# Performance work log

Hardware: AMD Instinct MI355X
Metric: run time of the kernel (lower is better)

The kernel has to match this reference:

```python
import jax, jax.numpy as jnp
import numpy as np

B = 64        # batch
N = 1024      # num_nodes
D_IN = 2      # input feature dim per node
U = 64        # num_units (hidden)
K = 2         # max_diffusion_step


def setup_inputs() -> dict:
    key = jax.random.key(0)
    ks = jax.random.split(key, 8)
    inputs = jax.random.normal(ks[0], (B, N * D_IN), dtype=jnp.float32)
    hx = jax.random.normal(ks[1], (B, N * U), dtype=jnp.float32)
    # random-walk style supports: nonnegative, row-normalized -> stable Chebyshev recursion
    a0 = jax.random.uniform(ks[2], (N, N), dtype=jnp.float32)
    a1 = jax.random.uniform(ks[3], (N, N), dtype=jnp.float32)
    support0 = a0 / jnp.sum(a0, axis=1, keepdims=True)
    support1 = a1 / jnp.sum(a1, axis=1, keepdims=True)
    num_matrices = 2 * K + 1            # len(supports)*K + 1 = 5
    in_sz = (D_IN + U) * num_matrices   # 330
    # xavier-normal init
    std_o = float(np.sqrt(2.0 / (in_sz + 2 * U)))
    std_u = float(np.sqrt(2.0 / (in_sz + U)))
    weights_output = jax.random.normal(ks[4], (in_sz, 2 * U), dtype=jnp.float32) * std_o
    weights_update = jax.random.normal(ks[5], (in_sz, U), dtype=jnp.float32) * std_u
    biases_output = jnp.ones((2 * U,), dtype=jnp.float32)
    biases_update = jnp.zeros((U,), dtype=jnp.float32)
    return {"inputs": inputs, "hx": hx, "support0": support0, "support1": support1,
            "weights_output": weights_output, "biases_output": biases_output,
            "weights_update": weights_update, "biases_update": biases_update}


def _gconv(x_cat, supports, W, b, out_size):
    # x_cat: [B, N, F]  -> Chebyshev diffusion series then dense projection
    Bsz, Nn, F = x_cat.shape
    x0 = x_cat.transpose(1, 2, 0).reshape(Nn, F * Bsz)  # [N, F*B]
    xs = [x0]
    for S in supports:
        x1 = S @ x0
        xs.append(x1)
        xk1, xk2 = x1, x0
        for _ in range(2, K + 1):
            x2 = 2.0 * (S @ xk1) - xk2
            xs.append(x2)
            xk1, xk2 = x2, xk1
    M = len(xs)                                         # num_matrices
    x = jnp.stack(xs, axis=0)                           # [M, N, F*B]
    x = x.reshape(M, Nn, F, Bsz).transpose(3, 1, 2, 0)  # [B, N, F, M]
    x = x.reshape(Bsz * Nn, F * M)
    y = x @ W + b                                       # [B*N, out_size]
    return y.reshape(Bsz, Nn * out_size)


def reference(inputs, hx, support0, support1, weights_output, biases_output,
              weights_update, biases_update):
    supports = (support0, support1)
    xi = inputs.reshape(B, N, D_IN)
    hs = hx.reshape(B, N, U)
    cat = jnp.concatenate([xi, hs], axis=2)             # [B, N, D_IN+U]
    value = jax.nn.sigmoid(_gconv(cat, supports, weights_output, biases_output, 2 * U))
    value = value.reshape(B, N, 2 * U)
    r = value[..., :U].reshape(B, N * U)
    u = value[..., U:].reshape(B, N * U)
    cat2 = jnp.concatenate([xi, (r * hx).reshape(B, N, U)], axis=2)
    c = jnp.tanh(_gconv(cat2, supports, weights_update, biases_update, U))
    return u * hx + (1.0 - u) * c
```

## Files before the change

kernel.cpp:

```cpp
#include <hip/hip_runtime.h>


typedef unsigned short u16;
typedef unsigned int u32;
typedef short s16x8 __attribute__((ext_vector_type(8)));
typedef float f32x4 __attribute__((ext_vector_type(4)));
typedef u16 u16x4 __attribute__((ext_vector_type(4)));

#define NN 1024
#define NB 64
#define NF 66
#define NCOLS 4224
#define KPAD 352
#define ASTRIDE 360

__device__ __forceinline__ u16 f2bf(float f) {
  u32 u = __builtin_bit_cast(u32, f);
  u = (u + 0x7fffu + ((u >> 16) & 1u)) >> 16;
  return (u16)u;
}
__device__ __forceinline__ float bf2f(u16 h) {
  u32 u = ((u32)h) << 16;
  return __builtin_bit_cast(float, u);
}

__device__ __forceinline__ void gload16(const void* g, void* l) {
  __builtin_amdgcn_global_load_lds(
      (const __attribute__((address_space(1))) u32*)g,
      (__attribute__((address_space(3))) u32*)l, 16, 0, 0);
}

#define CHEB_WAIT(N)                                   \
  do {                                                 \
    asm volatile("s_waitcnt vmcnt(" #N ")" ::: "memory"); \
    __builtin_amdgcn_s_barrier();                      \
    asm volatile("" ::: "memory");                     \
  } while (0)


__global__ __launch_bounds__(256) void pack_supports(
    const float* __restrict__ s0, const float* __restrict__ s1,
    u16* __restrict__ d0, u16* __restrict__ d1) {
  int i = (blockIdx.x * 256 + threadIdx.x) * 4;
  f32x4 a = *(const f32x4*)(s0 + i);
  f32x4 b = *(const f32x4*)(s1 + i);
  u16x4 oa, ob;
  oa.x = f2bf(a.x); oa.y = f2bf(a.y); oa.z = f2bf(a.z); oa.w = f2bf(a.w);
  ob.x = f2bf(b.x); ob.y = f2bf(b.y); ob.z = f2bf(b.z); ob.w = f2bf(b.w);
  *(u16x4*)(d0 + i) = oa;
  *(u16x4*)(d1 + i) = ob;
}

__global__ __launch_bounds__(64) void pack_w(
    const float* __restrict__ W, u16* __restrict__ Wt, int ldo) {
  int o = blockIdx.y;
  int kp = blockIdx.x * 64 + threadIdx.x;
  if (kp >= KPAD) return;
  float v = 0.f;
  if (kp < 330) {
    int m = kp / 66;
    int f = kp - m * 66;
    v = W[(f * 5 + m) * ldo + o];
  }
  Wt[(size_t)o * KPAD + kp] = f2bf(v);
}

__global__ __launch_bounds__(256) void pack_x0_inputs(
    const float* __restrict__ inp, u16* __restrict__ x0t, u16* __restrict__ x0pt) {
  int b = blockIdx.x, t = threadIdx.x;
  int n4 = t * 4;
  const float* src = inp + b * 2048 + n4 * 2;
  f32x4 a = *(const f32x4*)src;
  f32x4 c = *(const f32x4*)(src + 4);
  u16x4 r0, r1;
  r0.x = f2bf(a.x); r0.y = f2bf(a.z); r0.z = f2bf(c.x); r0.w = f2bf(c.z);
  r1.x = f2bf(a.y); r1.y = f2bf(a.w); r1.z = f2bf(c.y); r1.w = f2bf(c.w);
  size_t o0 = (size_t)(b)*NN + n4;
  size_t o1 = (size_t)(64 + b) * NN + n4;
  *(u16x4*)(x0t + o0) = r0;  *(u16x4*)(x0t + o1) = r1;
  *(u16x4*)(x0pt + o0) = r0; *(u16x4*)(x0pt + o1) = r1;
}

__global__ __launch_bounds__(256) void pack_x0_hx(
    const float* __restrict__ hx, u16* __restrict__ x0t) {
  __shared__ float tile[64][65];
  int n0 = blockIdx.x * 64, b = blockIdx.y, t = threadIdx.x;
  int u4 = (t & 15) * 4, r0 = t >> 4;
#pragma unroll
  for (int p = 0; p < 4; p++) {
    int row = p * 16 + r0;
    f32x4 v = *(const f32x4*)(hx + ((size_t)b << 16) + (size_t)(n0 + row) * 64 + u4);
    tile[row][u4] = v.x; tile[row][u4 + 1] = v.y;
    tile[row][u4 + 2] = v.z; tile[row][u4 + 3] = v.w;
  }
  __syncthreads();
  int n4 = (t & 15) * 4, uu0 = t >> 4;
#pragma unroll
  for (int p = 0; p < 4; p++) {
    int u = p * 16 + uu0;
    u16x4 o;
    o.x = f2bf(tile[n4][u]);     o.y = f2bf(tile[n4 + 1][u]);
    o.z = f2bf(tile[n4 + 2][u]); o.w = f2bf(tile[n4 + 3][u]);
    *(u16x4*)&x0t[(size_t)((2 + u) * 64 + b) * NN + n0 + n4] = o;
  }
}


__global__ __launch_bounds__(256, 3) void cheb_gemm(
    const u16* __restrict__ S0, const u16* __restrict__ S1,
    const u16* __restrict__ Xi0, const u16* __restrict__ Xi1,
    u16* __restrict__ Xo0, u16* __restrict__ Xo1,
    const u16* __restrict__ Xprev, int use_prev) {
  __shared__ u16 As[3][128 * 32];
  __shared__ u16 Bs[3][128 * 32];
  const int t = threadIdx.x;
  const int lane = t & 63;
  const int w = t >> 6;

  const int lid = blockIdx.x;
  const int work = (lid & 7) * 66 + (lid >> 3);
  const int y = work & 7;
  const int tt = work >> 3;
  const int x = tt % 33;
  const int z = tt / 33;
  const int n0 = x * 128;
  const int m0 = y * 128;
  const u16* S = z ? S1 : S0;
  const u16* Xi = z ? Xi1 : Xi0;
  u16* Xo = z ? Xo1 : Xo0;

  const int swz = ((lane & 3) ^ ((lane >> 3) & 3)) * 8;
  const int rl = lane >> 2;
  const u16* pA0 = S + (size_t)(m0 + w * 32 + rl) * NN + swz;
  const u16* pA1 = pA0 + (size_t)16 * NN;
  const u16* pB0 = Xi + (size_t)(n0 + w * 32 + rl) * NN + swz;
  const u16* pB1 = pB0 + (size_t)16 * NN;
  const int db0 = (w * 32) * 32;
  const int db1 = (w * 32 + 16) * 32;

  const int wm = (w >> 1) * 64;
  const int wn = (w & 1) * 64;
  const int fr = lane & 15;
  const int q = lane >> 4;
  const int fo = (q ^ ((fr >> 1) & 3)) * 8;

  f32x4 acc[4][4];
#pragma unroll
  for (int i = 0; i < 4; i++)
#pragma unroll
    for (int j = 0; j < 4; j++) acc[i][j] = f32x4{0.f, 0.f, 0.f, 0.f};

  auto stage = [&](u16* dA, u16* dB) {
    gload16(pA0, dA + db0);
    gload16(pA1, dA + db1);
    gload16(pB0, dB + db0);
    gload16(pB1, dB + db1);
    pA0 += 32; pA1 += 32; pB0 += 32; pB1 += 32;
  };
  auto compute = [&](const u16* cA, const u16* cB) {
    s16x8 af[4], bfr[4];
#pragma unroll
    for (int i = 0; i < 4; i++)
      af[i] = *(const s16x8*)&cA[(wm + i * 16 + fr) * 32 + fo];
#pragma unroll
    for (int j = 0; j < 4; j++)
      bfr[j] = *(const s16x8*)&cB[(wn + j * 16 + fr) * 32 + fo];
#pragma unroll
    for (int i = 0; i < 4; i++)
#pragma unroll
      for (int j = 0; j < 4; j++)
        acc[i][j] = __builtin_amdgcn_mfma_f32_16x16x32_bf16(af[i], bfr[j], acc[i][j], 0, 0, 0);
  };

  u16* a0 = &As[0][0]; u16* a1 = &As[1][0]; u16* a2 = &As[2][0];
  u16* b0 = &Bs[0][0]; u16* b1 = &Bs[1][0]; u16* b2 = &Bs[2][0];

  stage(a0, b0);
  stage(a1, b1);
#pragma unroll 1
  for (int it = 0; it < 10; it++) {
    CHEB_WAIT(4); stage(a2, b2); compute(a0, b0);
    CHEB_WAIT(4); stage(a0, b0); compute(a1, b1);
    CHEB_WAIT(4); stage(a1, b1); compute(a2, b2);
  }
  CHEB_WAIT(4); compute(a0, b0);
  CHEB_WAIT(0); compute(a1, b1);

  const int nr0 = (lane >> 4) << 2;
#pragma unroll
  for (int i = 0; i < 4; i++) {
    const int node = m0 + wm + i * 16 + nr0;
#pragma unroll
    for (int j = 0; j < 4; j++) {
      const int colg = n0 + wn + j * 16 + fr;
      size_t off = (size_t)colg * NN + node;
      f32x4 c = acc[i][j];
      if (use_prev) {
        u16x4 p = *(const u16x4*)&Xprev[off];
        c.x = 2.f * c.x - bf2f(p.x);
        c.y = 2.f * c.y - bf2f(p.y);
        c.z = 2.f * c.z - bf2f(p.z);
        c.w = 2.f * c.w - bf2f(p.w);
      }
      u16x4 o;
      o.x = f2bf(c.x); o.y = f2bf(c.y); o.z = f2bf(c.z); o.w = f2bf(c.w);
      *(u16x4*)&Xo[off] = o;
    }
  }
}


__device__ __forceinline__ void proj_stage(
    u16* A, const u16* __restrict__ X0, const u16* __restrict__ X1,
    const u16* __restrict__ X2, const u16* __restrict__ X3,
    const u16* __restrict__ X4, int b, int n0, int t) {
  for (int idx = t; idx < 1408; idx += 256) {
    const int kp0 = (idx >> 4) * 4;
    const int n4 = (idx & 15) * 4;
    u16x4 v[4];
#pragma unroll
    for (int r = 0; r < 4; r++) {
      const int kp = kp0 + r;
      if (kp < 330) {
        const int m = kp / 66;
        const int f = kp - m * 66;
        const u16* Xm = m == 0 ? X0 : m == 1 ? X1 : m == 2 ? X2 : m == 3 ? X3 : X4;
        v[r] = *(const u16x4*)(Xm + (size_t)(f * 64 + b) * NN + n0 + n4);
      } else {
        v[r] = u16x4{0, 0, 0, 0};
      }
    }
#pragma unroll
    for (int c = 0; c < 4; c++) {
      u16x4 o;
      o.x = v[0][c]; o.y = v[1][c]; o.z = v[2][c]; o.w = v[3][c];
      *(u16x4*)&A[(n4 + c) * ASTRIDE + kp0] = o;
    }
  }
}

__global__ __launch_bounds__(256) void proj1(
    const u16* __restrict__ X0, const u16* __restrict__ X1, const u16* __restrict__ X2,
    const u16* __restrict__ X3, const u16* __restrict__ X4,
    const u16* __restrict__ Wt, const float* __restrict__ bias,
    const float* __restrict__ hx, u16* __restrict__ X0p, float* __restrict__ uout) {
  __shared__ u16 A[64 * ASTRIDE];
  const int t = threadIdx.x;
  const int n0 = blockIdx.x * 64;
  const int b = blockIdx.y;
  proj_stage(A, X0, X1, X2, X3, X4, b, n0, t);
  __syncthreads();

  const int lane = t & 63;
  const int w = t >> 6;
  const int fr = lane & 15;
  const int q8 = (lane >> 4) * 8;
  const u16* arow = &A[(w * 16 + fr) * ASTRIDE + q8];

  f32x4 acc[8];
#pragma unroll
  for (int j = 0; j < 8; j++) acc[j] = f32x4{0.f, 0.f, 0.f, 0.f};

  for (int kc = 0; kc < KPAD; kc += 32) {
    const s16x8 af = *(const s16x8*)(arow + kc);
#pragma unroll
    for (int j = 0; j < 8; j++) {
      const s16x8 bf = *(const s16x8*)&Wt[(size_t)(j * 16 + fr) * KPAD + kc + q8];
      acc[j] = __builtin_amdgcn_mfma_f32_16x16x32_bf16(af, bf, acc[j], 0, 0, 0);
    }
  }

  const int nl0 = (lane >> 4) * 4;
  const int n = n0 + w * 16 + nl0;
#pragma unroll
  for (int j = 0; j < 8; j++) {
    const int o = j * 16 + fr;
    const float bs = bias[o];
    f32x4 v;
    v.x = 1.f / (1.f + __expf(-(acc[j].x + bs)));
    v.y = 1.f / (1.f + __expf(-(acc[j].y + bs)));
    v.z = 1.f / (1.f + __expf(-(acc[j].z + bs)));
    v.w = 1.f / (1.f + __expf(-(acc[j].w + bs)));
    if (o < 64) {
      const float* hxp = hx + ((size_t)b << 16) + (size_t)n * 64 + o;
      u16x4 s;
      s.x = f2bf(v.x * hxp[0 * 64]);
      s.y = f2bf(v.y * hxp[1 * 64]);
      s.z = f2bf(v.z * hxp[2 * 64]);
      s.w = f2bf(v.w * hxp[3 * 64]);
      *(u16x4*)&X0p[(size_t)((2 + o) * 64 + b) * NN + n] = s;
    } else {
      float* up = uout + (((size_t)b << 10) + n) * 64 + (o - 64);
      up[0 * 64] = v.x; up[1 * 64] = v.y; up[2 * 64] = v.z; up[3 * 64] = v.w;
    }
  }
}

__global__ __launch_bounds__(256) void proj2(
    const u16* __restrict__ X0, const u16* __restrict__ X1, const u16* __restrict__ X2,
    const u16* __restrict__ X3, const u16* __restrict__ X4,
    const u16* __restrict__ Wt, const float* __restrict__ bias,
    const float* __restrict__ hx, const float* uin, float* out) {
  __shared__ u16 A[64 * ASTRIDE];
  const int t = threadIdx.x;
  const int n0 = blockIdx.x * 64;
  const int b = blockIdx.y;
  proj_stage(A, X0, X1, X2, X3, X4, b, n0, t);
  __syncthreads();

  const int lane = t & 63;
  const int w = t >> 6;
  const int fr = lane & 15;
  const int q8 = (lane >> 4) * 8;
  const u16* arow = &A[(w * 16 + fr) * ASTRIDE + q8];

  f32x4 acc[4];
#pragma unroll
  for (int j = 0; j < 4; j++) acc[j] = f32x4{0.f, 0.f, 0.f, 0.f};

  for (int kc = 0; kc < KPAD; kc += 32) {
    const s16x8 af = *(const s16x8*)(arow + kc);
#pragma unroll
    for (int j = 0; j < 4; j++) {
      const s16x8 bf = *(const s16x8*)&Wt[(size_t)(j * 16 + fr) * KPAD + kc + q8];
      acc[j] = __builtin_amdgcn_mfma_f32_16x16x32_bf16(af, bf, acc[j], 0, 0, 0);
    }
  }

  const int nl0 = (lane >> 4) * 4;
  const int n = n0 + w * 16 + nl0;
#pragma unroll
  for (int j = 0; j < 4; j++) {
    const int o = j * 16 + fr;
    const float bs = bias[o];
    const size_t base = (((size_t)b << 10) + n) * 64 + o;
    float c0 = tanhf(acc[j].x + bs);
    float c1 = tanhf(acc[j].y + bs);
    float c2 = tanhf(acc[j].z + bs);
    float c3 = tanhf(acc[j].w + bs);
    float u0 = uin[base + 0 * 64], u1 = uin[base + 1 * 64];
    float u2 = uin[base + 2 * 64], u3 = uin[base + 3 * 64];
    float h0 = hx[base + 0 * 64], h1 = hx[base + 1 * 64];
    float h2 = hx[base + 2 * 64], h3 = hx[base + 3 * 64];
    out[base + 0 * 64] = u0 * h0 + (1.f - u0) * c0;
    out[base + 1 * 64] = u1 * h1 + (1.f - u1) * c1;
    out[base + 2 * 64] = u2 * h2 + (1.f - u2) * c2;
    out[base + 3 * 64] = u3 * h3 + (1.f - u3) * c3;
  }
}


extern "C" void kernel_launch(void* const* d_in, const int* in_sizes, int n_in,
                              void* d_out, int out_size, void* d_ws, size_t ws_size,
                              hipStream_t stream) {
  (void)in_sizes; (void)n_in; (void)out_size; (void)ws_size;
  const float* inp = (const float*)d_in[0];
  const float* hx  = (const float*)d_in[1];
  const float* s0  = (const float*)d_in[2];
  const float* s1  = (const float*)d_in[3];
  const float* Wo  = (const float*)d_in[4];
  const float* bo  = (const float*)d_in[5];
  const float* Wu  = (const float*)d_in[6];
  const float* bu  = (const float*)d_in[7];
  float* out = (float*)d_out;

  char* p = (char*)d_ws;
  u16* Sb0 = (u16*)p; p += (size_t)NN * NN * 2;
  u16* Sb1 = (u16*)p; p += (size_t)NN * NN * 2;
  const size_t xbytes = (size_t)NCOLS * NN * 2;
  u16* X0T = (u16*)p; p += xbytes;
  u16* X1T = (u16*)p; p += xbytes;
  u16* X2T = (u16*)p; p += xbytes;
  u16* X3T = (u16*)p; p += xbytes;
  u16* X4T = (u16*)p; p += xbytes;
  u16* X0P = (u16*)p; p += xbytes;
  u16* Wt1 = (u16*)p; p += (size_t)128 * KPAD * 2;
  u16* Wt2 = (u16*)p; p += (size_t)64 * KPAD * 2;

  pack_supports<<<dim3(1024), dim3(256), 0, stream>>>(s0, s1, Sb0, Sb1);
  pack_w<<<dim3(6, 128), dim3(64), 0, stream>>>(Wo, Wt1, 128);
  pack_w<<<dim3(6, 64), dim3(64), 0, stream>>>(Wu, Wt2, 64);
  pack_x0_inputs<<<dim3(64), dim3(256), 0, stream>>>(inp, X0T, X0P);
  pack_x0_hx<<<dim3(16, 64), dim3(256), 0, stream>>>(hx, X0T);
  cheb_gemm<<<dim3(528), dim3(256), 0, stream>>>(Sb0, Sb1, X0T, X0T, X1T, X3T,
                                                 (const u16*)nullptr, 0);
  cheb_gemm<<<dim3(528), dim3(256), 0, stream>>>(Sb0, Sb1, X1T, X3T, X2T, X4T, X0T, 1);
  proj1<<<dim3(16, 64), dim3(256), 0, stream>>>(X0T, X1T, X2T, X3T, X4T, Wt1, bo, hx, X0P, out);
  cheb_gemm<<<dim3(528), dim3(256), 0, stream>>>(Sb0, Sb1, X0P, X0P, X1T, X3T,
                                                 (const u16*)nullptr, 0);
  cheb_gemm<<<dim3(528), dim3(256), 0, stream>>>(Sb0, Sb1, X1T, X3T, X2T, X4T, X0P, 1);
  proj2<<<dim3(16, 64), dim3(256), 0, stream>>>(X0P, X1T, X2T, X3T, X4T, Wt2, bu, hx, out, out);
}
```

Baseline: 297.5 us.

## Precompute Chebyshev polynomial matrices and fuse diffusion into one stacked GEMM

Computes T2(S)=2S^2-I for each support once per call with a small square GEMM, stacks [S0; T2(S0); S1; T2(S1)] into a 4096x1024 matrix, and replaces the two dependent cheb_gemm launches per gconv with a single GEMM against X0. This removes one serial dependency and the Xprev read, and gives a larger single launch with a 4-stage load pipeline. In exchange it adds an N^3 GEMM for the support squares, rounds S^2 to bf16 before use, which changes numerics, and uses more LDS per block.

```diff
diff --git a/kernel.cpp b/kernel.cpp
--- a/kernel.cpp
+++ b/kernel.cpp
@@ -30,25 +30,45 @@
       (__attribute__((address_space(3))) u32*)l, 16, 0, 0);
 }
 
-#define CHEB_WAIT(N)                                   \
-  do {                                                 \
+#define CHEB_WAIT(N)                                      \
+  do {                                                    \
     asm volatile("s_waitcnt vmcnt(" #N ")" ::: "memory"); \
-    __builtin_amdgcn_s_barrier();                      \
-    asm volatile("" ::: "memory");                     \
+    __builtin_amdgcn_s_barrier();                         \
+    asm volatile("" ::: "memory");                        \
   } while (0)
 
 
 __global__ __launch_bounds__(256) void pack_supports(
     const float* __restrict__ s0, const float* __restrict__ s1,
-    u16* __restrict__ d0, u16* __restrict__ d1) {
-  int i = (blockIdx.x * 256 + threadIdx.x) * 4;
-  f32x4 a = *(const f32x4*)(s0 + i);
-  f32x4 b = *(const f32x4*)(s1 + i);
-  u16x4 oa, ob;
-  oa.x = f2bf(a.x); oa.y = f2bf(a.y); oa.z = f2bf(a.z); oa.w = f2bf(a.w);
-  ob.x = f2bf(b.x); ob.y = f2bf(b.y); ob.z = f2bf(b.z); ob.w = f2bf(b.w);
-  *(u16x4*)(d0 + i) = oa;
-  *(u16x4*)(d1 + i) = ob;
+    u16* __restrict__ Acat, u16* __restrict__ ST0, u16* __restrict__ ST1) {
+  __shared__ float tile[64][65];
+  const int z = blockIdx.y;
+  const float* S = z ? s1 : s0;
+  u16* ST = z ? ST1 : ST0;
+  const int r0 = (blockIdx.x >> 4) * 64, c0 = (blockIdx.x & 15) * 64;
+  const int t = threadIdx.x;
+  const size_t sbase = (size_t)z * 2048 * NN;
+  int cc4 = (t & 15) * 4, rr = t >> 4;
+#pragma unroll
+  for (int p = 0; p < 4; p++) {
+    int r = p * 16 + rr;
+    f32x4 v = *(const f32x4*)(S + (size_t)(r0 + r) * NN + c0 + cc4);
+    tile[r][cc4] = v.x; tile[r][cc4 + 1] = v.y;
+    tile[r][cc4 + 2] = v.z; tile[r][cc4 + 3] = v.w;
+    u16x4 o;
+    o.x = f2bf(v.x); o.y = f2bf(v.y); o.z = f2bf(v.z); o.w = f2bf(v.w);
+    *(u16x4*)&Acat[sbase + (size_t)(r0 + r) * NN + c0 + cc4] = o;
+  }
+  __syncthreads();
+  int rr4 = (t & 15) * 4, cc = t >> 4;
+#pragma unroll
+  for (int p = 0; p < 4; p++) {
+    int c = p * 16 + cc;
+    u16x4 o;
+    o.x = f2bf(tile[rr4][c]);     o.y = f2bf(tile[rr4 + 1][c]);
+    o.z = f2bf(tile[rr4 + 2][c]); o.w = f2bf(tile[rr4 + 3][c]);
+    *(u16x4*)&ST[(size_t)(c0 + c) * NN + r0 + rr4] = o;
+  }
 }
 
 __global__ __launch_bounds__(64) void pack_w(
@@ -106,58 +126,32 @@
 }
 
 
-__global__ __launch_bounds__(256, 3) void cheb_gemm(
-    const u16* __restrict__ S0, const u16* __restrict__ S1,
-    const u16* __restrict__ Xi0, const u16* __restrict__ Xi1,
-    u16* __restrict__ Xo0, u16* __restrict__ Xo1,
-    const u16* __restrict__ Xprev, int use_prev) {
-  __shared__ u16 As[3][128 * 32];
-  __shared__ u16 Bs[3][128 * 32];
-  const int t = threadIdx.x;
-  const int lane = t & 63;
-  const int w = t >> 6;
-
-  const int lid = blockIdx.x;
-  const int work = (lid & 7) * 66 + (lid >> 3);
-  const int y = work & 7;
-  const int tt = work >> 3;
-  const int x = tt % 33;
-  const int z = tt / 33;
-  const int n0 = x * 128;
-  const int m0 = y * 128;
-  const u16* S = z ? S1 : S0;
-  const u16* Xi = z ? Xi1 : Xi0;
-  u16* Xo = z ? Xo1 : Xo0;
-
-  const int swz = ((lane & 3) ^ ((lane >> 3) & 3)) * 8;
-  const int rl = lane >> 2;
-  const u16* pA0 = S + (size_t)(m0 + w * 32 + rl) * NN + swz;
-  const u16* pA1 = pA0 + (size_t)16 * NN;
-  const u16* pB0 = Xi + (size_t)(n0 + w * 32 + rl) * NN + swz;
-  const u16* pB1 = pB0 + (size_t)16 * NN;
+__device__ __forceinline__ void gemm128_pipe(
+    const u16* pAr, const u16* pBr,
+    u16* As, u16* Bs,
+    int w, int lane, f32x4 acc[4][4]) {
   const int db0 = (w * 32) * 32;
   const int db1 = (w * 32 + 16) * 32;
-
+  const u16* pA0 = pAr; const u16* pA1 = pAr + (size_t)16 * NN;
+  const u16* pB0 = pBr; const u16* pB1 = pBr + (size_t)16 * NN;
   const int wm = (w >> 1) * 64;
   const int wn = (w & 1) * 64;
   const int fr = lane & 15;
   const int q = lane >> 4;
   const int fo = (q ^ ((fr >> 1) & 3)) * 8;
 
-  f32x4 acc[4][4];
-#pragma unroll
-  for (int i = 0; i < 4; i++)
-#pragma unroll
-    for (int j = 0; j < 4; j++) acc[i][j] = f32x4{0.f, 0.f, 0.f, 0.f};
-
-  auto stage = [&](u16* dA, u16* dB) {
+  auto stage = [&](int buf) {
+    u16* dA = As + buf * (128 * 32);
+    u16* dB = Bs + buf * (128 * 32);
     gload16(pA0, dA + db0);
     gload16(pA1, dA + db1);
     gload16(pB0, dB + db0);
     gload16(pB1, dB + db1);
     pA0 += 32; pA1 += 32; pB0 += 32; pB1 += 32;
   };
-  auto compute = [&](const u16* cA, const u16* cB) {
+  auto compute = [&](int buf) {
+    const u16* cA = As + buf * (128 * 32);
+    const u16* cB = Bs + buf * (128 * 32);
     s16x8 af[4], bfr[4];
 #pragma unroll
     for (int i = 0; i < 4; i++)
@@ -172,20 +166,55 @@
         acc[i][j] = __builtin_amdgcn_mfma_f32_16x16x32_bf16(af[i], bfr[j], acc[i][j], 0, 0, 0);
   };
 
-  u16* a0 = &As[0][0]; u16* a1 = &As[1][0]; u16* a2 = &As[2][0];
-  u16* b0 = &Bs[0][0]; u16* b1 = &Bs[1][0]; u16* b2 = &Bs[2][0];
-
-  stage(a0, b0);
-  stage(a1, b1);
+  stage(0); stage(1); stage(2);
 #pragma unroll 1
-  for (int it = 0; it < 10; it++) {
-    CHEB_WAIT(4); stage(a2, b2); compute(a0, b0);
-    CHEB_WAIT(4); stage(a0, b0); compute(a1, b1);
-    CHEB_WAIT(4); stage(a1, b1); compute(a2, b2);
-  }
-  CHEB_WAIT(4); compute(a0, b0);
-  CHEB_WAIT(0); compute(a1, b1);
-
+  for (int it = 0; it < 7; it++) {
+    CHEB_WAIT(8); stage(3); compute(0);
+    CHEB_WAIT(8); stage(0); compute(1);
+    CHEB_WAIT(8); stage(1); compute(2);
+    CHEB_WAIT(8); stage(2); compute(3);
+  }
+  CHEB_WAIT(8); stage(3); compute(0);
+  CHEB_WAIT(8); compute(1);
+  CHEB_WAIT(4); compute(2);
+  CHEB_WAIT(0); compute(3);
+}
+
+__global__ __launch_bounds__(256, 2) void gconv_gemm(
+    const u16* __restrict__ Acat, const u16* __restrict__ Bx,
+    u16* __restrict__ X1, u16* __restrict__ X2,
+    u16* __restrict__ X3, u16* __restrict__ X4) {
+  __shared__ u16 As[4][128 * 32];
+  __shared__ u16 Bs[4][128 * 32];
+  const int t = threadIdx.x;
+  const int lane = t & 63;
+  const int w = t >> 6;
+
+  const int lid = blockIdx.x;
+  const int work = (lid & 7) * 132 + (lid >> 3);
+  const int mt = work / 33;
+  const int nt = work % 33;
+
+  const int rl = lane >> 2;
+  const int swz = ((lane & 3) ^ ((lane >> 3) & 3)) * 8;
+  const u16* pAr = Acat + (size_t)(mt * 128 + w * 32 + rl) * NN + swz;
+  const u16* pBr = Bx + (size_t)(nt * 128 + w * 32 + rl) * NN + swz;
+
+  f32x4 acc[4][4];
+#pragma unroll
+  for (int i = 0; i < 4; i++)
+#pragma unroll
+    for (int j = 0; j < 4; j++) acc[i][j] = f32x4{0.f, 0.f, 0.f, 0.f};
+
+  gemm128_pipe(pAr, pBr, &As[0][0], &Bs[0][0], w, lane, acc);
+
+  const int md = mt >> 3;
+  u16* Xo = md == 0 ? X1 : md == 1 ? X2 : md == 2 ? X3 : X4;
+  const int m0 = (mt & 7) * 128;
+  const int n0 = nt * 128;
+  const int wm = (w >> 1) * 64;
+  const int wn = (w & 1) * 64;
+  const int fr = lane & 15;
   const int nr0 = (lane >> 4) << 2;
 #pragma unroll
   for (int i = 0; i < 4; i++) {
@@ -193,18 +222,62 @@
 #pragma unroll
     for (int j = 0; j < 4; j++) {
       const int colg = n0 + wn + j * 16 + fr;
-      size_t off = (size_t)colg * NN + node;
       f32x4 c = acc[i][j];
-      if (use_prev) {
-        u16x4 p = *(const u16x4*)&Xprev[off];
-        c.x = 2.f * c.x - bf2f(p.x);
-        c.y = 2.f * c.y - bf2f(p.y);
-        c.z = 2.f * c.z - bf2f(p.z);
-        c.w = 2.f * c.w - bf2f(p.w);
-      }
       u16x4 o;
       o.x = f2bf(c.x); o.y = f2bf(c.y); o.z = f2bf(c.z); o.w = f2bf(c.w);
-      *(u16x4*)&Xo[off] = o;
+      *(u16x4*)&Xo[(size_t)colg * NN + node] = o;
+    }
+  }
+}
+
+__global__ __launch_bounds__(256, 2) void sq_gemm(
+    const u16* __restrict__ ST0, const u16* __restrict__ ST1, u16* Acat) {
+  __shared__ u16 As[4][128 * 32];
+  __shared__ u16 Bs[4][128 * 32];
+  const int t = threadIdx.x;
+  const int lane = t & 63;
+  const int w = t >> 6;
+
+  const int lid = blockIdx.x;
+  const int work = (lid & 7) * 16 + (lid >> 3);
+  const int z = work >> 6;
+  const int rr = work & 63;
+  const int mtile = rr >> 3, ntile = rr & 7;
+
+  const u16* A = z ? ST1 : ST0;
+  const u16* B = Acat + (size_t)(z * 2048) * NN;
+
+  const int rl = lane >> 2;
+  const int swz = ((lane & 3) ^ ((lane >> 3) & 3)) * 8;
+  const u16* pAr = A + (size_t)(mtile * 128 + w * 32 + rl) * NN + swz;
+  const u16* pBr = B + (size_t)(ntile * 128 + w * 32 + rl) * NN + swz;
+
+  f32x4 acc[4][4];
+#pragma unroll
+  for (int i = 0; i < 4; i++)
+#pragma unroll
+    for (int j = 0; j < 4; j++) acc[i][j] = f32x4{0.f, 0.f, 0.f, 0.f};
+
+  gemm128_pipe(pAr, pBr, &As[0][0], &Bs[0][0], w, lane, acc);
+
+  const size_t tbase = z ? 3072 : 1024;
+  const int wm = (w >> 1) * 64;
+  const int wn = (w & 1) * 64;
+  const int fr = lane & 15;
+  const int nr0 = (lane >> 4) << 2;
+#pragma unroll
+  for (int i = 0; i < 4; i++) {
+    const int node = mtile * 128 + wm + i * 16 + nr0;
+#pragma unroll
+    for (int j = 0; j < 4; j++) {
+      const int colg = ntile * 128 + wn + j * 16 + fr;
+      f32x4 c = acc[i][j];
+      u16x4 o;
+      o.x = f2bf(2.f * c.x - (float)(node + 0 == colg));
+      o.y = f2bf(2.f * c.y - (float)(node + 1 == colg));
+      o.z = f2bf(2.f * c.z - (float)(node + 2 == colg));
+      o.w = f2bf(2.f * c.w - (float)(node + 3 == colg));
+      *(u16x4*)&Acat[(tbase + (size_t)colg) * NN + node] = o;
     }
   }
 }
@@ -365,8 +438,9 @@
   float* out = (float*)d_out;
 
   char* p = (char*)d_ws;
-  u16* Sb0 = (u16*)p; p += (size_t)NN * NN * 2;
-  u16* Sb1 = (u16*)p; p += (size_t)NN * NN * 2;
+  u16* Acat = (u16*)p; p += (size_t)4096 * NN * 2;
+  u16* ST0  = (u16*)p; p += (size_t)NN * NN * 2;
+  u16* ST1  = (u16*)p; p += (size_t)NN * NN * 2;
   const size_t xbytes = (size_t)NCOLS * NN * 2;
   u16* X0T = (u16*)p; p += xbytes;
   u16* X1T = (u16*)p; p += xbytes;
@@ -377,17 +451,14 @@
   u16* Wt1 = (u16*)p; p += (size_t)128 * KPAD * 2;
   u16* Wt2 = (u16*)p; p += (size_t)64 * KPAD * 2;
 
-  pack_supports<<<dim3(1024), dim3(256), 0, stream>>>(s0, s1, Sb0, Sb1);
+  pack_supports<<<dim3(256, 2), dim3(256), 0, stream>>>(s0, s1, Acat, ST0, ST1);
+  sq_gemm<<<dim3(128), dim3(256), 0, stream>>>(ST0, ST1, Acat);
   pack_w<<<dim3(6, 128), dim3(64), 0, stream>>>(Wo, Wt1, 128);
   pack_w<<<dim3(6, 64), dim3(64), 0, stream>>>(Wu, Wt2, 64);
   pack_x0_inputs<<<dim3(64), dim3(256), 0, stream>>>(inp, X0T, X0P);
   pack_x0_hx<<<dim3(16, 64), dim3(256), 0, stream>>>(hx, X0T);
-  cheb_gemm<<<dim3(528), dim3(256), 0, stream>>>(Sb0, Sb1, X0T, X0T, X1T, X3T,
-                                                 (const u16*)nullptr, 0);
-  cheb_gemm<<<dim3(528), dim3(256), 0, stream>>>(Sb0, Sb1, X1T, X3T, X2T, X4T, X0T, 1);
+  gconv_gemm<<<dim3(1056), dim3(256), 0, stream>>>(Acat, X0T, X1T, X2T, X3T, X4T);
   proj1<<<dim3(16, 64), dim3(256), 0, stream>>>(X0T, X1T, X2T, X3T, X4T, Wt1, bo, hx, X0P, out);
-  cheb_gemm<<<dim3(528), dim3(256), 0, stream>>>(Sb0, Sb1, X0P, X0P, X1T, X3T,
-                                                 (const u16*)nullptr, 0);
-  cheb_gemm<<<dim3(528), dim3(256), 0, stream>>>(Sb0, Sb1, X1T, X3T, X2T, X4T, X0P, 1);
+  gconv_gemm<<<dim3(1056), dim3(256), 0, stream>>>(Acat, X0P, X1T, X2T, X3T, X4T);
   proj2<<<dim3(16, 64), dim3(256), 0, stream>>>(X0P, X1T, X2T, X3T, X4T, Wt2, bu, hx, out, out);
 }
```

Result: slower. 320.4 us (+7.7%).
